# Kernel tuning notes

Hardware: AMD Instinct MI355X
Metric: run time of the kernel (lower is better)

Reference implementation:

```python
import jax, jax.numpy as jnp
import numpy as np
from jax import lax

K = 3
K2 = K * K
EPS = 1e-5


def conv3x3(x, w, b=None):
    # x [B,C,H,W], w [O,C,3,3], padding=1, stride=1
    out = lax.conv_general_dilated(x, w, (1, 1), [(1, 1), (1, 1)],
                                   dimension_numbers=('NCHW', 'OIHW', 'NCHW'))
    if b is not None:
        out = out + b[None, :, None, None]
    return out


def deform_conv(x, w_off, b_off, w_mod, b_mod, w):
    # DCNv2-style deformable conv, k=3, stride=1, pad=1, dilation=1, no bias.
    B, C, H, W = x.shape
    O = w.shape[0]
    off = conv3x3(x, w_off, b_off).reshape(B, K2, 2, H, W)   # (dy,dx) per tap
    mod = 2.0 * jax.nn.sigmoid(conv3x3(x, w_mod, b_mod))      # [B,9,H,W]
    dy, dx = off[:, :, 0], off[:, :, 1]

    ky = (jnp.arange(K) - 1).astype(x.dtype)
    base_y = jnp.repeat(ky, K)   # [9]
    base_x = jnp.tile(ky, K)     # [9]
    ii = jnp.arange(H, dtype=x.dtype)[:, None]
    jj = jnp.arange(W, dtype=x.dtype)[None, :]
    py = ii[None, None] + base_y[None, :, None, None] + dy   # [B,9,H,W]
    px = jj[None, None] + base_x[None, :, None, None] + dx

    def sample(xb, pyb, pxb):
        # xb [C,H,W]; pyb/pxb [9,H,W] -> [C,9,H,W], bilinear w/ zero pad
        y0 = jnp.floor(pyb)
        x0 = jnp.floor(pxb)
        wy = pyb - y0
        wx = pxb - x0
        flat = xb.reshape(C, -1)
        acc = jnp.zeros((C, K2, H, W), xb.dtype)
        for yc, xc, wt in ((y0, x0, (1 - wy) * (1 - wx)),
                           (y0, x0 + 1, (1 - wy) * wx),
                           (y0 + 1, x0, wy * (1 - wx)),
                           (y0 + 1, x0 + 1, wy * wx)):
            yi = yc.astype(jnp.int32)
            xi = xc.astype(jnp.int32)
            valid = (yi >= 0) & (yi < H) & (xi >= 0) & (xi < W)
            idx = (jnp.clip(yi, 0, H - 1) * W + jnp.clip(xi, 0, W - 1)).reshape(-1)
            g = jnp.take(flat, idx, axis=1).reshape(C, K2, H, W)
            acc = acc + g * (wt * valid)[None]
        return acc

    patches = jax.vmap(sample)(x, py, px)          # [B,C,9,H,W]
    patches = patches * mod[:, None]               # modulated
    return jnp.einsum('bckhw,ock->bohw', patches, w.reshape(O, C, K2))


def bn_relu(x):
    # BatchNorm2d(affine=False), train-mode batch stats, biased variance
    mean = jnp.mean(x, axis=(0, 2, 3), keepdims=True)
    var = jnp.mean(jnp.square(x - mean), axis=(0, 2, 3), keepdims=True)
    return jax.nn.relu((x - mean) * lax.rsqrt(var + EPS))


def maxpool2(x):
    return lax.reduce_window(x, -jnp.inf, lax.max, (1, 1, 2, 2), (1, 1, 2, 2), 'VALID')


def setup_inputs() -> dict:
    key = jax.random.key(0)
    ks = jax.random.split(key, 11)
    B, Cin, Cout, H, W = 4, 64, 128, 128, 128
    std1 = 1.0 / np.sqrt(Cin * K2)
    std2 = 1.0 / np.sqrt(Cout * K2)
    return {
        'x': jax.random.normal(ks[0], (B, Cin, H, W), jnp.float32),
        'w_off1': jax.random.normal(ks[1], (2 * K2, Cin, K, K), jnp.float32) * 0.01,
        'b_off1': jax.random.normal(ks[2], (2 * K2,), jnp.float32) * 0.01,
        'w_mod1': jax.random.normal(ks[3], (K2, Cin, K, K), jnp.float32) * 0.01,
        'b_mod1': jnp.zeros((K2,), jnp.float32),
        'w1': jax.random.normal(ks[4], (Cout, Cin, K, K), jnp.float32) * std1,
        'w_off2': jax.random.normal(ks[5], (2 * K2, Cout, K, K), jnp.float32) * 0.01,
        'b_off2': jax.random.normal(ks[6], (2 * K2,), jnp.float32) * 0.01,
        'w_mod2': jax.random.normal(ks[7], (K2, Cout, K, K), jnp.float32) * 0.01,
        'b_mod2': jnp.zeros((K2,), jnp.float32),
        'w2': jax.random.normal(ks[8], (Cout, Cout, K, K), jnp.float32) * std2,
    }


def reference(x, w_off1, b_off1, w_mod1, b_mod1, w1,
              w_off2, b_off2, w_mod2, b_mod2, w2):
    h = bn_relu(deform_conv(x, w_off1, b_off1, w_mod1, b_mod1, w1))
    h = bn_relu(deform_conv(h, w_off2, b_off2, w_mod2, b_mod2, w2))
    return maxpool2(h)
```

## Files before the change

### kernel.cpp

```cpp
#include <hip/hip_runtime.h>
#include <math.h>

#define HH 128
#define WW 128
#define HWSZ 16384

typedef __attribute__((ext_vector_type(8))) _Float16 h8;
typedef __attribute__((ext_vector_type(2))) _Float16 h2;
typedef __attribute__((ext_vector_type(4))) float f32x4;
typedef __attribute__((ext_vector_type(2))) float f32x2;
typedef unsigned short ushort;

__device__ __forceinline__ ushort f2h(float f) {
    _Float16 h = (_Float16)f;
    ushort u;
    __builtin_memcpy(&u, &h, 2);
    return u;
}
__device__ __forceinline__ unsigned f2h2(float lo, float hi) {
    h2 r;
    r.x = (_Float16)lo;
    r.y = (_Float16)hi;
    unsigned u;
    __builtin_memcpy(&u, &r, 4);
    return u;
}
__device__ __forceinline__ f32x2 unpk_h2(unsigned u) {
    h2 h;
    __builtin_memcpy(&h, &u, 4);
    return (f32x2){(float)h.x, (float)h.y};
}

__global__ __launch_bounds__(256) void prep_weights(
    const float* __restrict__ w1, const float* __restrict__ w2,
    const float* __restrict__ w_off1, const float* __restrict__ w_mod1,
    const float* __restrict__ w_off2, const float* __restrict__ w_mod2,
    ushort* __restrict__ Wt1, ushort* __restrict__ Wt2,
    ushort* __restrict__ Wo1, ushort* __restrict__ Wo2) {
    int bid = blockIdx.x, tid = threadIdx.x;
    if (bid < 336) {
        int i = bid * 256 + tid;
        int o = i / 672, kq = i % 672;
        int k = kq / 72, c = kq % 72;
        float v = (k < 9 && c < 64) ? w1[(o * 64 + c) * 9 + k] : 0.f;
        Wt1[i] = f2h(v);
    } else if (bid < 960) {
        int i = (bid - 336) * 256 + tid;
        int o = i / 1248, kq = i % 1248;
        int k = kq / 136, c = kq % 136;
        float v = (k < 9 && c < 128) ? w2[(o * 128 + c) * 9 + k] : 0.f;
        Wt2[i] = f2h(v);
    } else if (bid < 1032) {
        int i = (bid - 960) * 256 + tid;
        int o = i / 576, kap = i % 576;
        int k = kap / 64, c = kap % 64;
        float v = 0.f;
        if (o < 18) v = w_off1[(o * 64 + c) * 9 + k];
        else if (o < 27) v = w_mod1[((o - 18) * 64 + c) * 9 + k];
        Wo1[i] = f2h(v);
    } else {
        int i = (bid - 1032) * 256 + tid;
        int o = i / 1152, kap = i % 1152;
        int k = kap / 128, c = kap % 128;
        float v = 0.f;
        if (o < 18) v = w_off2[(o * 128 + c) * 9 + k];
        else if (o < 27) v = w_mod2[((o - 18) * 128 + c) * 9 + k];
        Wo2[i] = f2h(v);
    }
}

template <int C>
__global__ __launch_bounds__(256) void nhwc_cvt(const float* __restrict__ xin,
                                                unsigned* __restrict__ xout) {
    __shared__ float tile[64][C + 1];
    const int m0 = blockIdx.x * 64;
    const int b = m0 >> 14;
    const int hw0 = m0 & 16383;
    const int t = threadIdx.x;
    const int pr = t & 63, cr = t >> 6;
#pragma unroll
    for (int it = 0; it < C / 4; ++it) {
        int c = it * 4 + cr;
        tile[pr][c] = xin[(((size_t)(b * C + c)) << 14) + hw0 + pr];
    }
    __syncthreads();
    constexpr int CH = C / 2;
#pragma unroll
    for (int it = 0; it < 64 * CH / 256; ++it) {
        int slot = it * 256 + t;
        int p = slot / CH, cc = slot % CH;
        xout[(size_t)(m0 + p) * CH + cc] =
            f2h2(tile[p][2 * cc], tile[p][2 * cc + 1]);
    }
}

__global__ __launch_bounds__(256) void bn_apply_ew(
    const unsigned* __restrict__ xin, const float* __restrict__ praw,
    unsigned* __restrict__ xout) {
    __shared__ float lstats[256];
    if (threadIdx.x < 128) {
        int c = threadIdx.x;
        float s = 0.f, q = 0.f;
#pragma unroll
        for (int r = 0; r < 8; ++r) {
            s += praw[r * 256 + c];
            q += praw[r * 256 + 128 + c];
        }
        float mean = s / 65536.f;
        float var = q / 65536.f - mean * mean;
        lstats[c] = mean;
        lstats[128 + c] = rsqrtf(var + 1e-5f);
    }
    __syncthreads();
    int i = blockIdx.x * 256 + threadIdx.x;
    uint4 v = ((const uint4*)xin)[i];
    int c0 = ((i * 4) & 63) * 2;
    unsigned ov[4];
    unsigned in[4] = {v.x, v.y, v.z, v.w};
#pragma unroll
    for (int d = 0; d < 4; ++d) {
        int c = c0 + 2 * d;
        f32x2 f = unpk_h2(in[d]);
        float a = fmaxf(0.f, (f.x - lstats[c]) * lstats[128 + c]);
        float b2 = fmaxf(0.f, (f.y - lstats[c + 1]) * lstats[128 + c + 1]);
        ov[d] = f2h2(a, b2);
    }
    ((uint4*)xout)[i] = uint4{ov[0], ov[1], ov[2], ov[3]};
}

template <int C>
__global__ __launch_bounds__(256) void offmod_nhwc(
    const ushort* __restrict__ xh, const ushort* __restrict__ wt,
    const float* __restrict__ b_off, const float* __restrict__ b_mod,
    float* __restrict__ dyb, float* __restrict__ dxb, float* __restrict__ mob,
    float* __restrict__ praw) {
    constexpr int K = C * 9;
    if (blockIdx.x < 8) praw[blockIdx.x * 256 + threadIdx.x] = 0.f;
    const int m0 = blockIdx.x * 64;
    const int b = m0 >> 14;
    const int hw0 = m0 & 16383;
    const int h = hw0 >> 7;
    const int w0 = hw0 & 127;
    const int tid = threadIdx.x;
    const int lane = tid & 63, wv = tid >> 6;
    const int n16 = lane & 15, quad = lane >> 4;
    const int p = wv * 16 + n16;
    const int w = w0 + p;

    int tbase[9];
    bool tval[9];
#pragma unroll
    for (int k = 0; k < 9; ++k) {
        int yy = h + k / 3 - 1, xx = w + k % 3 - 1;
        tval[k] = ((unsigned)yy < 128u) && ((unsigned)xx < 128u);
        int cy = min(max(yy, 0), 127), cx = min(max(xx, 0), 127);
        tbase[k] = ((b << 14) + (cy << 7) + cx) * C + quad * 8;
    }

    f32x4 acc[2];
    acc[0] = (f32x4){0.f, 0.f, 0.f, 0.f};
    acc[1] = (f32x4){0.f, 0.f, 0.f, 0.f};

    const ushort* b0p = wt + (size_t)n16 * K + quad * 8;
    const ushort* b1p = wt + (size_t)(16 + n16) * K + quad * 8;

#pragma unroll
    for (int s = 0; s < K / 32; ++s) {
        const int k = (s * 32) / C;
        const int c0 = (s * 32) % C;
        h8 a = {0, 0, 0, 0, 0, 0, 0, 0};
        if (tval[k]) a = *(const h8*)(xh + (size_t)tbase[k] + c0);
        const h8 bv0 = *(const h8*)(b0p + s * 32);
        const h8 bv1 = *(const h8*)(b1p + s * 32);
        acc[0] = __builtin_amdgcn_mfma_f32_16x16x32_f16(a, bv0, acc[0], 0, 0, 0);
        acc[1] = __builtin_amdgcn_mfma_f32_16x16x32_f16(a, bv1, acc[1], 0, 0, 0);
    }

    __shared__ float sm[32 * 65];
#pragma unroll
    for (int nt = 0; nt < 2; ++nt) {
        int n = nt * 16 + n16;
        int pb = wv * 16 + quad * 4;
#pragma unroll
        for (int r = 0; r < 4; ++r) sm[n * 65 + pb + r] = acc[nt][r];
    }
    __syncthreads();
    {
        int n = tid >> 3, i8 = tid & 7;
        if (n < 27) {
            const float* sp = sm + n * 65 + i8 * 8;
            int px = hw0 + i8 * 8;
            if (n < 18) {
                int k = n >> 1;
                float bias = b_off[n];
                float* dst =
                    ((n & 1) ? dxb : dyb) + (((size_t)(b * 9 + k)) << 14) + px;
#pragma unroll
                for (int j = 0; j < 8; j += 4) {
                    float4 v = make_float4(sp[j] + bias, sp[j + 1] + bias,
                                           sp[j + 2] + bias, sp[j + 3] + bias);
                    *(float4*)(dst + j) = v;
                }
            } else {
                float bias = b_mod[n - 18];
                float* dst = mob + (((size_t)(b * 9 + (n - 18))) << 14) + px;
#pragma unroll
                for (int j = 0; j < 8; j += 4) {
                    float4 v;
                    v.x = 2.f / (1.f + expf(-(sp[j] + bias)));
                    v.y = 2.f / (1.f + expf(-(sp[j + 1] + bias)));
                    v.z = 2.f / (1.f + expf(-(sp[j + 2] + bias)));
                    v.w = 2.f / (1.f + expf(-(sp[j + 3] + bias)));
                    *(float4*)(dst + j) = v;
                }
            }
        }
    }
}

template <int C>
__global__ __launch_bounds__(256) void deform_mfma3(
    const ushort* __restrict__ xh, const float* __restrict__ dyb,
    const float* __restrict__ dxb, const float* __restrict__ mob,
    const ushort* __restrict__ wt, unsigned* __restrict__ xout,
    float* __restrict__ praw) {
    constexpr int PIX = 32;
    constexpr int AST = C + 8;
    constexpr int CPW = C + 8;
    constexpr int KP = ((9 * CPW + 31) / 32) * 32;
    constexpr int NCC = C / 8;
    constexpr int NIT = PIX * NCC / 256;
    constexpr int ABUF = PIX * AST;

    __shared__ __align__(16) char smem_raw[2 * ABUF * 2 + PIX * 9 * 32];
    ushort* abuf0 = (ushort*)smem_raw;
    ushort* abuf1 = abuf0 + ABUF;
    int* tb = (int*)(abuf0 + 2 * ABUF);
    float* tw = (float*)(tb + PIX * 9 * 4);

    const int m0 = blockIdx.x * PIX;
    const int b = m0 >> 14;
    const int hw0 = m0 & 16383;
    const int h = hw0 >> 7, w0 = hw0 & 127;
    const int tid = threadIdx.x;

    for (int r = tid; r < PIX * 9; r += 256) {
        int p = r & (PIX - 1), k = r / PIX;
        int oi = ((b * 9 + k) << 14) + hw0 + p;
        float py = (float)(h + k / 3 - 1) + dyb[oi];
        float px = (float)(w0 + p + k % 3 - 1) + dxb[oi];
        float mv = mob[oi];
        float y0f = floorf(py), x0f = floorf(px);
        float wy = py - y0f, wx = px - x0f;
        int y0 = (int)y0f, x0 = (int)x0f;
        int y1 = y0 + 1, x1 = x0 + 1;
        float f00 = (1.f - wy) * (1.f - wx) *
                    (((unsigned)y0 < 128u && (unsigned)x0 < 128u) ? mv : 0.f);
        float f01 = (1.f - wy) * wx *
                    (((unsigned)y0 < 128u && (unsigned)x1 < 128u) ? mv : 0.f);
        float f10 = wy * (1.f - wx) *
                    (((unsigned)y1 < 128u && (unsigned)x0 < 128u) ? mv : 0.f);
        float f11 = wy * wx *
                    (((unsigned)y1 < 128u && (unsigned)x1 < 128u) ? mv : 0.f);
        int cy0 = min(max(y0, 0), 127), cy1 = min(max(y1, 0), 127);
        int cx0 = min(max(x0, 0), 127), cx1 = min(max(x1, 0), 127);
        int bpx = b << 14;
        int s = (p * 9 + k) * 4;
        tb[s + 0] = (bpx + (cy0 << 7) + cx0) * C;
        tb[s + 1] = (bpx + (cy0 << 7) + cx1) * C;
        tb[s + 2] = (bpx + (cy1 << 7) + cx0) * C;
        tb[s + 3] = (bpx + (cy1 << 7) + cx1) * C;
        tw[s + 0] = f00;
        tw[s + 1] = f01;
        tw[s + 2] = f10;
        tw[s + 3] = f11;
    }
    __syncthreads();

    auto issue_loads = [&](int kc, uint4 (&q)[2][4], float4 (&fw)[2]) {
#pragma unroll
        for (int it = 0; it < NIT; ++it) {
            int e = it * 256 + tid;
            int p = e / NCC, cc = e % NCC;
            int s = (p * 9 + kc) * 4;
            int4 bi = *(const int4*)&tb[s];
            fw[it] = *(const float4*)&tw[s];
            q[it][0] = *(const uint4*)(xh + (size_t)bi.x + cc * 8);
            q[it][1] = *(const uint4*)(xh + (size_t)bi.y + cc * 8);
            q[it][2] = *(const uint4*)(xh + (size_t)bi.z + cc * 8);
            q[it][3] = *(const uint4*)(xh + (size_t)bi.w + cc * 8);
        }
    };
    auto interp_write = [&](ushort* dst, uint4 (&q)[2][4], float4 (&fw)[2]) {
#pragma unroll
        for (int it = 0; it < NIT; ++it) {
            int e = it * 256 + tid;
            int p = e / NCC, cc = e % NCC;
            _Float16 w0h = (_Float16)fw[it].x, w1h = (_Float16)fw[it].y;
            _Float16 w2h = (_Float16)fw[it].z, w3h = (_Float16)fw[it].w;
            h8 F0 = {w0h, w0h, w0h, w0h, w0h, w0h, w0h, w0h};
            h8 F1 = {w1h, w1h, w1h, w1h, w1h, w1h, w1h, w1h};
            h8 F2 = {w2h, w2h, w2h, w2h, w2h, w2h, w2h, w2h};
            h8 F3 = {w3h, w3h, w3h, w3h, w3h, w3h, w3h, w3h};
            h8 a0, a1, a2, a3;
            __builtin_memcpy(&a0, &q[it][0], 16);
            __builtin_memcpy(&a1, &q[it][1], 16);
            __builtin_memcpy(&a2, &q[it][2], 16);
            __builtin_memcpy(&a3, &q[it][3], 16);
            h8 v = a0 * F0 + a1 * F1 + a2 * F2 + a3 * F3;
            uint4 ov;
            __builtin_memcpy(&ov, &v, 16);
            *(uint4*)&dst[p * AST + cc * 8] = ov;
        }
    };

    {
        uint4 q[2][4];
        float4 fw[2];
        issue_loads(0, q, fw);
        interp_write(abuf0, q, fw);
    }
    __syncthreads();

    const int lane = tid & 63, wv = tid >> 6;
    const int n16 = lane & 15, quad = lane >> 4;

    f32x4 acc[2][2];
#pragma unroll
    for (int mt = 0; mt < 2; ++mt)
#pragma unroll
        for (int nt = 0; nt < 2; ++nt) acc[mt][nt] = (f32x4){0.f, 0.f, 0.f, 0.f};

    const ushort* bbase[2];
#pragma unroll
    for (int nt = 0; nt < 2; ++nt)
        bbase[nt] = wt + (size_t)(wv * 32 + nt * 16 + n16) * KP + quad * 8;

#pragma unroll 1
    for (int kc = 0; kc < 9; ++kc) {
        uint4 q[2][4];
        float4 fw[2];
        if (kc < 8) issue_loads(kc + 1, q, fw);

        const ushort* ab = (kc & 1) ? abuf1 : abuf0;
#pragma unroll
        for (int s = 0; s < C / 32; ++s) {
            h8 av[2], bv[2];
#pragma unroll
            for (int mt = 0; mt < 2; ++mt)
                av[mt] = *(const h8*)(ab + (mt * 16 + n16) * AST + s * 32 +
                                      quad * 8);
#pragma unroll
            for (int nt = 0; nt < 2; ++nt)
                bv[nt] = *(const h8*)(bbase[nt] + kc * CPW + s * 32);
#pragma unroll
            for (int mt = 0; mt < 2; ++mt)
#pragma unroll
                for (int nt = 0; nt < 2; ++nt)
                    acc[mt][nt] = __builtin_amdgcn_mfma_f32_16x16x32_f16(
                        av[mt], bv[nt], acc[mt][nt], 0, 0, 0);
        }
        if (kc < 8)
            interp_write((kc & 1) ? abuf0 : abuf1, q, fw);
        __syncthreads();
    }

    float* sm = (float*)smem_raw;
    constexpr int SROW = PIX + 1;
#pragma unroll
    for (int mt = 0; mt < 2; ++mt)
#pragma unroll
        for (int nt = 0; nt < 2; ++nt) {
            int o = wv * 32 + nt * 16 + n16;
            int mb = mt * 16 + quad * 4;
#pragma unroll
            for (int r = 0; r < 4; ++r) sm[o * SROW + mb + r] = acc[mt][nt][r];
        }
    __syncthreads();
    {
        int o = tid >> 1, half = tid & 1;
        const float* sp = sm + o * SROW + half * 16;
        float s = 0.f, qq = 0.f;
#pragma unroll
        for (int i = 0; i < 16; i += 4) {
            float4 v = make_float4(sp[i], sp[i + 1], sp[i + 2], sp[i + 3]);
            s += v.x + v.y + v.z + v.w;
            qq += v.x * v.x + v.y * v.y + v.z * v.z + v.w * v.w;
        }
        s += __shfl_down(s, 1, 64);
        qq += __shfl_down(qq, 1, 64);
        if (half == 0) {
            float* pr = praw + (blockIdx.x & 7) * 256;
            atomicAdd(&pr[o], s);
            atomicAdd(&pr[128 + o], qq);
        }
    }
    {
        int p = tid >> 3, cc8 = tid & 7;
        unsigned ov[8];
#pragma unroll
        for (int j = 0; j < 8; ++j) {
            int c = cc8 * 16 + 2 * j;
            ov[j] = f2h2(sm[c * SROW + p], sm[(c + 1) * SROW + p]);
        }
        uint4* dst = (uint4*)(xout + ((size_t)(m0 + p)) * 64 + cc8 * 8);
        dst[0] = uint4{ov[0], ov[1], ov[2], ov[3]};
        dst[1] = uint4{ov[4], ov[5], ov[6], ov[7]};
    }
}

template <int C>
__global__ __launch_bounds__(256) void deform_mfma3p(
    const ushort* __restrict__ xh, const float* __restrict__ dyb,
    const float* __restrict__ dxb, const float* __restrict__ mob,
    const ushort* __restrict__ wt, float* __restrict__ pout,
    float* __restrict__ praw) {
    constexpr int PIX = 32;
    constexpr int AST = C + 8;
    constexpr int CPW = C + 8;
    constexpr int KP = ((9 * CPW + 31) / 32) * 32;
    constexpr int NCC = C / 8;
    constexpr int NIT = PIX * NCC / 256;
    constexpr int ABUF = PIX * AST;

    __shared__ __align__(16) char smem_raw[2 * ABUF * 2 + PIX * 9 * 32];
    ushort* abuf0 = (ushort*)smem_raw;
    ushort* abuf1 = abuf0 + ABUF;
    int* tb = (int*)(abuf0 + 2 * ABUF);
    float* tw = (float*)(tb + PIX * 9 * 4);

    const int bid = blockIdx.x;
    const int b = bid >> 9;
    const int rp = (bid >> 3) & 63;
    const int g = bid & 7;
    const int tid = threadIdx.x;

    for (int r = tid; r < PIX * 9; r += 256) {
        int p = r & (PIX - 1), k = r / PIX;
        int row = 2 * rp + (p >> 4), col = g * 16 + (p & 15);
        int oi = ((b * 9 + k) << 14) + (row << 7) + col;
        float py = (float)(row + k / 3 - 1) + dyb[oi];
        float px = (float)(col + k % 3 - 1) + dxb[oi];
        float mv = mob[oi];
        float y0f = floorf(py), x0f = floorf(px);
        float wy = py - y0f, wx = px - x0f;
        int y0 = (int)y0f, x0 = (int)x0f;
        int y1 = y0 + 1, x1 = x0 + 1;
        float f00 = (1.f - wy) * (1.f - wx) *
                    (((unsigned)y0 < 128u && (unsigned)x0 < 128u) ? mv : 0.f);
        float f01 = (1.f - wy) * wx *
                    (((unsigned)y0 < 128u && (unsigned)x1 < 128u) ? mv : 0.f);
        float f10 = wy * (1.f - wx) *
                    (((unsigned)y1 < 128u && (unsigned)x0 < 128u) ? mv : 0.f);
        float f11 = wy * wx *
                    (((unsigned)y1 < 128u && (unsigned)x1 < 128u) ? mv : 0.f);
        int cy0 = min(max(y0, 0), 127), cy1 = min(max(y1, 0), 127);
        int cx0 = min(max(x0, 0), 127), cx1 = min(max(x1, 0), 127);
        int bpx = b << 14;
        int s = (p * 9 + k) * 4;
        tb[s + 0] = (bpx + (cy0 << 7) + cx0) * C;
        tb[s + 1] = (bpx + (cy0 << 7) + cx1) * C;
        tb[s + 2] = (bpx + (cy1 << 7) + cx0) * C;
        tb[s + 3] = (bpx + (cy1 << 7) + cx1) * C;
        tw[s + 0] = f00;
        tw[s + 1] = f01;
        tw[s + 2] = f10;
        tw[s + 3] = f11;
    }
    __syncthreads();

    auto issue_loads = [&](int kc, uint4 (&q)[2][4], float4 (&fw)[2]) {
#pragma unroll
        for (int it = 0; it < NIT; ++it) {
            int e = it * 256 + tid;
            int p = e / NCC, cc = e % NCC;
            int s = (p * 9 + kc) * 4;
            int4 bi = *(const int4*)&tb[s];
            fw[it] = *(const float4*)&tw[s];
            q[it][0] = *(const uint4*)(xh + (size_t)bi.x + cc * 8);
            q[it][1] = *(const uint4*)(xh + (size_t)bi.y + cc * 8);
            q[it][2] = *(const uint4*)(xh + (size_t)bi.z + cc * 8);
            q[it][3] = *(const uint4*)(xh + (size_t)bi.w + cc * 8);
        }
    };
    auto interp_write = [&](ushort* dst, uint4 (&q)[2][4], float4 (&fw)[2]) {
#pragma unroll
        for (int it = 0; it < NIT; ++it) {
            int e = it * 256 + tid;
            int p = e / NCC, cc = e % NCC;
            _Float16 w0h = (_Float16)fw[it].x, w1h = (_Float16)fw[it].y;
            _Float16 w2h = (_Float16)fw[it].z, w3h = (_Float16)fw[it].w;
            h8 F0 = {w0h, w0h, w0h, w0h, w0h, w0h, w0h, w0h};
            h8 F1 = {w1h, w1h, w1h, w1h, w1h, w1h, w1h, w1h};
            h8 F2 = {w2h, w2h, w2h, w2h, w2h, w2h, w2h, w2h};
            h8 F3 = {w3h, w3h, w3h, w3h, w3h, w3h, w3h, w3h};
            h8 a0, a1, a2, a3;
            __builtin_memcpy(&a0, &q[it][0], 16);
            __builtin_memcpy(&a1, &q[it][1], 16);
            __builtin_memcpy(&a2, &q[it][2], 16);
            __builtin_memcpy(&a3, &q[it][3], 16);
            h8 v = a0 * F0 + a1 * F1 + a2 * F2 + a3 * F3;
            uint4 ov;
            __builtin_memcpy(&ov, &v, 16);
            *(uint4*)&dst[p * AST + cc * 8] = ov;
        }
    };

    {
        uint4 q[2][4];
        float4 fw[2];
        issue_loads(0, q, fw);
        interp_write(abuf0, q, fw);
    }
    __syncthreads();

    const int lane = tid & 63, wv = tid >> 6;
    const int n16 = lane & 15, quad = lane >> 4;

    f32x4 acc[2][2];
#pragma unroll
    for (int mt = 0; mt < 2; ++mt)
#pragma unroll
        for (int nt = 0; nt < 2; ++nt) acc[mt][nt] = (f32x4){0.f, 0.f, 0.f, 0.f};

    const ushort* bbase[2];
#pragma unroll
    for (int nt = 0; nt < 2; ++nt)
        bbase[nt] = wt + (size_t)(wv * 32 + nt * 16 + n16) * KP + quad * 8;

#pragma unroll 1
    for (int kc = 0; kc < 9; ++kc) {
        uint4 q[2][4];
        float4 fw[2];
        if (kc < 8) issue_loads(kc + 1, q, fw);

        const ushort* ab = (kc & 1) ? abuf1 : abuf0;
#pragma unroll
        for (int s = 0; s < C / 32; ++s) {
            h8 av[2], bv[2];
#pragma unroll
            for (int mt = 0; mt < 2; ++mt)
                av[mt] = *(const h8*)(ab + (mt * 16 + n16) * AST + s * 32 +
                                      quad * 8);
#pragma unroll
            for (int nt = 0; nt < 2; ++nt)
                bv[nt] = *(const h8*)(bbase[nt] + kc * CPW + s * 32);
#pragma unroll
            for (int mt = 0; mt < 2; ++mt)
#pragma unroll
                for (int nt = 0; nt < 2; ++nt)
                    acc[mt][nt] = __builtin_amdgcn_mfma_f32_16x16x32_f16(
                        av[mt], bv[nt], acc[mt][nt], 0, 0, 0);
        }
        if (kc < 8)
            interp_write((kc & 1) ? abuf0 : abuf1, q, fw);
        __syncthreads();
    }

    float* sm = (float*)smem_raw;
    constexpr int SROW = PIX + 1;
#pragma unroll
    for (int mt = 0; mt < 2; ++mt)
#pragma unroll
        for (int nt = 0; nt < 2; ++nt) {
            int o = wv * 32 + nt * 16 + n16;
            int mb = mt * 16 + quad * 4;
#pragma unroll
            for (int r = 0; r < 4; ++r) sm[o * SROW + mb + r] = acc[mt][nt][r];
        }
    __syncthreads();
    {
        int o = tid >> 1, half = tid & 1;
        const float* so = sm + o * SROW;
        const float* sp = so + half * 16;
        float s = 0.f, qq = 0.f;
#pragma unroll
        for (int i = 0; i < 16; i += 4) {
            float4 v = make_float4(sp[i], sp[i + 1], sp[i + 2], sp[i + 3]);
            s += v.x + v.y + v.z + v.w;
            qq += v.x * v.x + v.y * v.y + v.z * v.z + v.w * v.w;
        }
        s += __shfl_down(s, 1, 64);
        qq += __shfl_down(qq, 1, 64);
        if (half == 0) {
            float* pr = praw + (blockIdx.x & 7) * 256;
            atomicAdd(&pr[o], s);
            atomicAdd(&pr[128 + o], qq);
        }
        float4 pv;
#pragma unroll
        for (int i = 0; i < 4; ++i) {
            int pc = half * 4 + i;
            float m0v = fmaxf(so[2 * pc], so[2 * pc + 1]);
            float m1v = fmaxf(so[16 + 2 * pc], so[16 + 2 * pc + 1]);
            ((float*)&pv)[i] = fmaxf(m0v, m1v);
        }
        *(float4*)(pout + (((size_t)(b * 128 + o)) << 12) + rp * 64 + g * 8 +
                   half * 4) = pv;
    }
}

__global__ __launch_bounds__(256) void pool_norm(const float* __restrict__ pout,
                                                 const float* __restrict__ praw,
                                                 float* __restrict__ out) {
    __shared__ float lstats[256];
    if (threadIdx.x < 128) {
        int c = threadIdx.x;
        float s = 0.f, q = 0.f;
#pragma unroll
        for (int r = 0; r < 8; ++r) {
            s += praw[r * 256 + c];
            q += praw[r * 256 + 128 + c];
        }
        float mean = s / 65536.f;
        float var = q / 65536.f - mean * mean;
        lstats[c] = mean;
        lstats[128 + c] = rsqrtf(var + 1e-5f);
    }
    __syncthreads();
    int i = blockIdx.x * 256 + threadIdx.x;
    int c = (i >> 10) & 127;
    float mean = lstats[c], rstd = lstats[128 + c];
    float4 v = ((const float4*)pout)[i];
    v.x = fmaxf(0.f, (v.x - mean) * rstd);
    v.y = fmaxf(0.f, (v.y - mean) * rstd);
    v.z = fmaxf(0.f, (v.z - mean) * rstd);
    v.w = fmaxf(0.f, (v.w - mean) * rstd);
    ((float4*)out)[i] = v;
}

extern "C" void kernel_launch(void* const* d_in, const int* in_sizes, int n_in,
                              void* d_out, int out_size, void* d_ws,
                              size_t ws_size, hipStream_t stream) {
    (void)in_sizes;
    (void)n_in;
    (void)out_size;
    (void)ws_size;
    const float* x = (const float*)d_in[0];
    const float* w_off1 = (const float*)d_in[1];
    const float* b_off1 = (const float*)d_in[2];
    const float* w_mod1 = (const float*)d_in[3];
    const float* b_mod1 = (const float*)d_in[4];
    const float* w1 = (const float*)d_in[5];
    const float* w_off2 = (const float*)d_in[6];
    const float* b_off2 = (const float*)d_in[7];
    const float* w_mod2 = (const float*)d_in[8];
    const float* b_mod2 = (const float*)d_in[9];
    const float* w2 = (const float*)d_in[10];
    float* out = (float*)d_out;
    float* ws = (float*)d_ws;

    ushort* Wt1 = (ushort*)ws;
    ushort* Wt2 = (ushort*)(ws + 43008);
    ushort* Wo1 = (ushort*)(ws + 43008 + 79872);
    ushort* Wo2 = (ushort*)(ws + 43008 + 79872 + 16384);
    float* dyb = ws + 172032;
    float* dxb = dyb + 589824;
    float* mob = dxb + 589824;
    float* hbuf = mob + 589824;
    float* xhf = hbuf + 8388608;
    float* h1hf = xhf + 2097152;
    float* praw = h1hf + 4194304;
    ushort* xh = (ushort*)xhf;
    ushort* h1h = (ushort*)h1hf;

    prep_weights<<<1176, 256, 0, stream>>>(w1, w2, w_off1, w_mod1, w_off2,
                                           w_mod2, Wt1, Wt2, Wo1, Wo2);

    nhwc_cvt<64><<<1024, 256, 0, stream>>>(x, (unsigned*)xh);
    offmod_nhwc<64><<<1024, 256, 0, stream>>>(xh, Wo1, b_off1, b_mod1, dyb, dxb,
                                              mob, praw);
    deform_mfma3<64><<<2048, 256, 0, stream>>>(xh, dyb, dxb, mob, Wt1,
                                               (unsigned*)hbuf, praw);
    bn_apply_ew<<<4096, 256, 0, stream>>>((const unsigned*)hbuf, praw,
                                          (unsigned*)h1h);

    offmod_nhwc<128><<<1024, 256, 0, stream>>>(h1h, Wo2, b_off2, b_mod2, dyb,
                                               dxb, mob, praw);
    deform_mfma3p<128><<<2048, 256, 0, stream>>>(h1h, dyb, dxb, mob, Wt2, hbuf,
                                                 praw);
    pool_norm<<<2048, 256, 0, stream>>>(hbuf, praw, out);
}
```

Measured before the change: 276.7 us.

## Double pixel tile per block, compress gather tables, swizzle LDS, split pipeline

Both deformable-conv MFMA kernels now process 64 pixels per block instead of 32, so each wave issues 4x2 MFMA tiles and reuses each weight fragment across twice as many rows. The launch grid halves to match. The per-tap gather table shrinks to one packed base offset with neighbour flags plus fp16-packed bilinear weights. LDS padding is replaced by an XOR swizzle. The gather/interpolate stage is split into two halves interleaved with the MFMA halves to overlap global loads with compute. This costs more registers and LDS per block, under a launch bound of 4 blocks per CU, and the weights now lose precision earlier by being stored as fp16.

```diff
diff --git a/kernel.cpp b/kernel.cpp
--- a/kernel.cpp
+++ b/kernel.cpp
@@ -219,33 +219,41 @@
 }
 
 template <int C>
-__global__ __launch_bounds__(256) void deform_mfma3(
+__global__ __launch_bounds__(256, 4) void deform_mfma3(
     const ushort* __restrict__ xh, const float* __restrict__ dyb,
     const float* __restrict__ dxb, const float* __restrict__ mob,
     const ushort* __restrict__ wt, unsigned* __restrict__ xout,
     float* __restrict__ praw) {
-    constexpr int PIX = 32;
-    constexpr int AST = C + 8;
+    constexpr int PIX = 64;
+    constexpr int NCH = C / 8;
+    constexpr int NCC = C / 8;
+    constexpr int NIT = PIX * NCC / 256;
+    constexpr int HNIT = NIT / 2;
+    constexpr int SH = (C / 32) / 2 > 0 ? (C / 32) / 2 : 1;
     constexpr int CPW = C + 8;
     constexpr int KP = ((9 * CPW + 31) / 32) * 32;
-    constexpr int NCC = C / 8;
-    constexpr int NIT = PIX * NCC / 256;
-    constexpr int ABUF = PIX * AST;
-
-    __shared__ __align__(16) char smem_raw[2 * ABUF * 2 + PIX * 9 * 32];
+    constexpr int ABUF = PIX * C;
+    constexpr int LOOPB = 2 * ABUF * 2 + PIX * 9 * 4 + PIX * 9 * 8;
+    constexpr int EPIB = 128 * (PIX + 1) * 4;
+    constexpr int SMEMB = LOOPB > EPIB ? LOOPB : EPIB;
+
+    __shared__ __align__(16) char smem_raw[SMEMB];
     ushort* abuf0 = (ushort*)smem_raw;
     ushort* abuf1 = abuf0 + ABUF;
-    int* tb = (int*)(abuf0 + 2 * ABUF);
-    float* tw = (float*)(tb + PIX * 9 * 4);
+    int* tbl = (int*)(abuf0 + 2 * ABUF);
+    unsigned* twl = (unsigned*)(smem_raw + 2 * ABUF * 2 + PIX * 9 * 4);
 
     const int m0 = blockIdx.x * PIX;
     const int b = m0 >> 14;
     const int hw0 = m0 & 16383;
     const int h = hw0 >> 7, w0 = hw0 & 127;
     const int tid = threadIdx.x;
+    const int lane = tid & 63, wv = tid >> 6;
+    const int n16 = lane & 15, quad = lane >> 4;
+    const int xr = n16 & (NCH - 1);
 
     for (int r = tid; r < PIX * 9; r += 256) {
-        int p = r & (PIX - 1), k = r / PIX;
+        int p = r & (PIX - 1), k = r >> 6;
         int oi = ((b * 9 + k) << 14) + hw0 + p;
         float py = (float)(h + k / 3 - 1) + dyb[oi];
         float px = (float)(w0 + p + k % 3 - 1) + dxb[oi];
@@ -264,70 +272,63 @@
                     (((unsigned)y1 < 128u && (unsigned)x1 < 128u) ? mv : 0.f);
         int cy0 = min(max(y0, 0), 127), cy1 = min(max(y1, 0), 127);
         int cx0 = min(max(x0, 0), 127), cx1 = min(max(x1, 0), 127);
-        int bpx = b << 14;
-        int s = (p * 9 + k) * 4;
-        tb[s + 0] = (bpx + (cy0 << 7) + cx0) * C;
-        tb[s + 1] = (bpx + (cy0 << 7) + cx1) * C;
-        tb[s + 2] = (bpx + (cy1 << 7) + cx0) * C;
-        tb[s + 3] = (bpx + (cy1 << 7) + cx1) * C;
-        tw[s + 0] = f00;
-        tw[s + 1] = f01;
-        tw[s + 2] = f10;
-        tw[s + 3] = f11;
-    }
-    __syncthreads();
-
-    auto issue_loads = [&](int kc, uint4 (&q)[2][4], float4 (&fw)[2]) {
-#pragma unroll
-        for (int it = 0; it < NIT; ++it) {
-            int e = it * 256 + tid;
+        int base00 = (((b << 14) + (cy0 << 7) + cx0)) * C;
+        int flags = ((cy1 != cy0) ? 2 : 0) | ((cx1 != cx0) ? 1 : 0);
+        int s = p * 9 + k;
+        tbl[s] = base00 | flags;
+        twl[2 * s] = f2h2(f00, f01);
+        twl[2 * s + 1] = f2h2(f10, f11);
+    }
+    __syncthreads();
+
+    auto issue_loads = [&](int kc, int it0, uint4 (&q)[HNIT][4],
+                           uint2 (&fw)[HNIT]) {
+#pragma unroll
+        for (int j = 0; j < HNIT; ++j) {
+            int e = (it0 + j) * 256 + tid;
             int p = e / NCC, cc = e % NCC;
-            int s = (p * 9 + kc) * 4;
-            int4 bi = *(const int4*)&tb[s];
-            fw[it] = *(const float4*)&tw[s];
-            q[it][0] = *(const uint4*)(xh + (size_t)bi.x + cc * 8);
-            q[it][1] = *(const uint4*)(xh + (size_t)bi.y + cc * 8);
-            q[it][2] = *(const uint4*)(xh + (size_t)bi.z + cc * 8);
-            q[it][3] = *(const uint4*)(xh + (size_t)bi.w + cc * 8);
+            int s = p * 9 + kc;
+            int ent = tbl[s];
+            fw[j] = *(const uint2*)&twl[2 * s];
+            int base = ent & ~3;
+            int dxo = (ent & 1) ? C : 0;
+            int dyo = (ent & 2) ? (C << 7) : 0;
+            const ushort* pp = xh + (size_t)base + cc * 8;
+            q[j][0] = *(const uint4*)(pp);
+            q[j][1] = *(const uint4*)(pp + dxo);
+            q[j][2] = *(const uint4*)(pp + dyo);
+            q[j][3] = *(const uint4*)(pp + dyo + dxo);
         }
     };
-    auto interp_write = [&](ushort* dst, uint4 (&q)[2][4], float4 (&fw)[2]) {
-#pragma unroll
-        for (int it = 0; it < NIT; ++it) {
-            int e = it * 256 + tid;
+    auto interp_write = [&](ushort* dst, int it0, uint4 (&q)[HNIT][4],
+                            uint2 (&fw)[HNIT]) {
+#pragma unroll
+        for (int j = 0; j < HNIT; ++j) {
+            int e = (it0 + j) * 256 + tid;
             int p = e / NCC, cc = e % NCC;
-            _Float16 w0h = (_Float16)fw[it].x, w1h = (_Float16)fw[it].y;
-            _Float16 w2h = (_Float16)fw[it].z, w3h = (_Float16)fw[it].w;
-            h8 F0 = {w0h, w0h, w0h, w0h, w0h, w0h, w0h, w0h};
-            h8 F1 = {w1h, w1h, w1h, w1h, w1h, w1h, w1h, w1h};
-            h8 F2 = {w2h, w2h, w2h, w2h, w2h, w2h, w2h, w2h};
-            h8 F3 = {w3h, w3h, w3h, w3h, w3h, w3h, w3h, w3h};
+            h2 w01, w23;
+            __builtin_memcpy(&w01, &fw[j].x, 4);
+            __builtin_memcpy(&w23, &fw[j].y, 4);
+            h8 F0 = {w01.x, w01.x, w01.x, w01.x, w01.x, w01.x, w01.x, w01.x};
+            h8 F1 = {w01.y, w01.y, w01.y, w01.y, w01.y, w01.y, w01.y, w01.y};
+            h8 F2 = {w23.x, w23.x, w23.x, w23.x, w23.x, w23.x, w23.x, w23.x};
+            h8 F3 = {w23.y, w23.y, w23.y, w23.y, w23.y, w23.y, w23.y, w23.y};
             h8 a0, a1, a2, a3;
-            __builtin_memcpy(&a0, &q[it][0], 16);
-            __builtin_memcpy(&a1, &q[it][1], 16);
-            __builtin_memcpy(&a2, &q[it][2], 16);
-            __builtin_memcpy(&a3, &q[it][3], 16);
+            __builtin_memcpy(&a0, &q[j][0], 16);
+            __builtin_memcpy(&a1, &q[j][1], 16);
+            __builtin_memcpy(&a2, &q[j][2], 16);
+            __builtin_memcpy(&a3, &q[j][3], 16);
             h8 v = a0 * F0 + a1 * F1 + a2 * F2 + a3 * F3;
             uint4 ov;
             __builtin_memcpy(&ov, &v, 16);
-            *(uint4*)&dst[p * AST + cc * 8] = ov;
+            int ccs = cc ^ (p & (NCH - 1));
+            *(uint4*)&dst[p * C + ccs * 8] = ov;
         }
     };
 
-    {
-        uint4 q[2][4];
-        float4 fw[2];
-        issue_loads(0, q, fw);
-        interp_write(abuf0, q, fw);
-    }
-    __syncthreads();
-
-    const int lane = tid & 63, wv = tid >> 6;
-    const int n16 = lane & 15, quad = lane >> 4;
-
-    f32x4 acc[2][2];
-#pragma unroll
-    for (int mt = 0; mt < 2; ++mt)
+    f32x4 acc[4][2];
+#pragma unroll
+    for (int mt = 0; mt < 4; ++mt)
 #pragma unroll
         for (int nt = 0; nt < 2; ++nt) acc[mt][nt] = (f32x4){0.f, 0.f, 0.f, 0.f};
 
@@ -336,39 +337,57 @@
     for (int nt = 0; nt < 2; ++nt)
         bbase[nt] = wt + (size_t)(wv * 32 + nt * 16 + n16) * KP + quad * 8;
 
-#pragma unroll 1
-    for (int kc = 0; kc < 9; ++kc) {
-        uint4 q[2][4];
-        float4 fw[2];
-        if (kc < 8) issue_loads(kc + 1, q, fw);
-
-        const ushort* ab = (kc & 1) ? abuf1 : abuf0;
-#pragma unroll
-        for (int s = 0; s < C / 32; ++s) {
-            h8 av[2], bv[2];
-#pragma unroll
-            for (int mt = 0; mt < 2; ++mt)
-                av[mt] = *(const h8*)(ab + (mt * 16 + n16) * AST + s * 32 +
-                                      quad * 8);
+    auto mfma_run = [&](const ushort* ab, int kc, int s0, int s1) {
+#pragma unroll
+        for (int s = s0; s < s1; ++s) {
+            h8 av[4], bv[2];
+            int ch = (s * 4 + quad) ^ xr;
+#pragma unroll
+            for (int mt = 0; mt < 4; ++mt)
+                av[mt] = *(const h8*)(ab + (mt * 16 + n16) * C + ch * 8);
 #pragma unroll
             for (int nt = 0; nt < 2; ++nt)
                 bv[nt] = *(const h8*)(bbase[nt] + kc * CPW + s * 32);
 #pragma unroll
-            for (int mt = 0; mt < 2; ++mt)
+            for (int mt = 0; mt < 4; ++mt)
 #pragma unroll
                 for (int nt = 0; nt < 2; ++nt)
                     acc[mt][nt] = __builtin_amdgcn_mfma_f32_16x16x32_f16(
                         av[mt], bv[nt], acc[mt][nt], 0, 0, 0);
         }
-        if (kc < 8)
-            interp_write((kc & 1) ? abuf0 : abuf1, q, fw);
+    };
+
+    {
+        uint4 q[HNIT][4];
+        uint2 fw[HNIT];
+        issue_loads(0, 0, q, fw);
+        interp_write(abuf0, 0, q, fw);
+        issue_loads(0, HNIT, q, fw);
+        interp_write(abuf0, HNIT, q, fw);
+    }
+    __syncthreads();
+
+#pragma unroll 1
+    for (int kc = 0; kc < 9; ++kc) {
+        const ushort* ab = (kc & 1) ? abuf1 : abuf0;
+        ushort* dst = (kc & 1) ? abuf0 : abuf1;
+        uint4 q[HNIT][4];
+        uint2 fw[HNIT];
+        if (kc < 8) issue_loads(kc + 1, 0, q, fw);
+        mfma_run(ab, kc, 0, SH);
+        if (kc < 8) {
+            interp_write(dst, 0, q, fw);
+            issue_loads(kc + 1, HNIT, q, fw);
+        }
+        mfma_run(ab, kc, SH, C / 32);
+        if (kc < 8) interp_write(dst, HNIT, q, fw);
         __syncthreads();
     }
 
     float* sm = (float*)smem_raw;
     constexpr int SROW = PIX + 1;
 #pragma unroll
-    for (int mt = 0; mt < 2; ++mt)
+    for (int mt = 0; mt < 4; ++mt)
 #pragma unroll
         for (int nt = 0; nt < 2; ++nt) {
             int o = wv * 32 + nt * 16 + n16;
@@ -379,10 +398,10 @@
     __syncthreads();
     {
         int o = tid >> 1, half = tid & 1;
-        const float* sp = sm + o * SROW + half * 16;
+        const float* sp = sm + o * SROW + half * 32;
         float s = 0.f, qq = 0.f;
 #pragma unroll
-        for (int i = 0; i < 16; i += 4) {
+        for (int i = 0; i < 32; i += 4) {
             float4 v = make_float4(sp[i], sp[i + 1], sp[i + 2], sp[i + 3]);
             s += v.x + v.y + v.z + v.w;
             qq += v.x * v.x + v.y * v.y + v.z * v.z + v.w * v.w;
@@ -396,48 +415,58 @@
         }
     }
     {
-        int p = tid >> 3, cc8 = tid & 7;
-        unsigned ov[8];
-#pragma unroll
-        for (int j = 0; j < 8; ++j) {
-            int c = cc8 * 16 + 2 * j;
+        int p = tid >> 2, cc4 = tid & 3;
+        unsigned ov[16];
+#pragma unroll
+        for (int j = 0; j < 16; ++j) {
+            int c = cc4 * 32 + 2 * j;
             ov[j] = f2h2(sm[c * SROW + p], sm[(c + 1) * SROW + p]);
         }
-        uint4* dst = (uint4*)(xout + ((size_t)(m0 + p)) * 64 + cc8 * 8);
+        uint4* dst = (uint4*)(xout + ((size_t)(m0 + p)) * 64 + cc4 * 16);
         dst[0] = uint4{ov[0], ov[1], ov[2], ov[3]};
         dst[1] = uint4{ov[4], ov[5], ov[6], ov[7]};
+        dst[2] = uint4{ov[8], ov[9], ov[10], ov[11]};
+        dst[3] = uint4{ov[12], ov[13], ov[14], ov[15]};
     }
 }
 
 template <int C>
-__global__ __launch_bounds__(256) void deform_mfma3p(
+__global__ __launch_bounds__(256, 4) void deform_mfma3p(
     const ushort* __restrict__ xh, const float* __restrict__ dyb,
     const float* __restrict__ dxb, const float* __restrict__ mob,
     const ushort* __restrict__ wt, float* __restrict__ pout,
     float* __restrict__ praw) {
-    constexpr int PIX = 32;
-    constexpr int AST = C + 8;
+    constexpr int PIX = 64;
+    constexpr int NCH = C / 8;
+    constexpr int NCC = C / 8;
+    constexpr int NIT = PIX * NCC / 256;
+    constexpr int HNIT = NIT / 2;
+    constexpr int SH = (C / 32) / 2 > 0 ? (C / 32) / 2 : 1;
     constexpr int CPW = C + 8;
     constexpr int KP = ((9 * CPW + 31) / 32) * 32;
-    constexpr int NCC = C / 8;
-    constexpr int NIT = PIX * NCC / 256;
-    constexpr int ABUF = PIX * AST;
-
-    __shared__ __align__(16) char smem_raw[2 * ABUF * 2 + PIX * 9 * 32];
+    constexpr int ABUF = PIX * C;
+    constexpr int LOOPB = 2 * ABUF * 2 + PIX * 9 * 4 + PIX * 9 * 8;
+    constexpr int EPIB = 128 * (PIX + 1) * 4;
+    constexpr int SMEMB = LOOPB > EPIB ? LOOPB : EPIB;
+
+    __shared__ __align__(16) char smem_raw[SMEMB];
     ushort* abuf0 = (ushort*)smem_raw;
     ushort* abuf1 = abuf0 + ABUF;
-    int* tb = (int*)(abuf0 + 2 * ABUF);
-    float* tw = (float*)(tb + PIX * 9 * 4);
+    int* tbl = (int*)(abuf0 + 2 * ABUF);
+    unsigned* twl = (unsigned*)(smem_raw + 2 * ABUF * 2 + PIX * 9 * 4);
 
     const int bid = blockIdx.x;
-    const int b = bid >> 9;
-    const int rp = (bid >> 3) & 63;
-    const int g = bid & 7;
+    const int b = bid >> 8;
+    const int rp = (bid >> 2) & 63;
+    const int g = bid & 3;
     const int tid = threadIdx.x;
+    const int lane = tid & 63, wv = tid >> 6;
+    const int n16 = lane & 15, quad = lane >> 4;
+    const int xr = n16 & (NCH - 1);
 
     for (int r = tid; r < PIX * 9; r += 256) {
-        int p = r & (PIX - 1), k = r / PIX;
-        int row = 2 * rp + (p >> 4), col = g * 16 + (p & 15);
+        int p = r & (PIX - 1), k = r >> 6;
+        int row = 2 * rp + (p >> 5), col = g * 32 + (p & 31);
         int oi = ((b * 9 + k) << 14) + (row << 7) + col;
         float py = (float)(row + k / 3 - 1) + dyb[oi];
         float px = (float)(col + k % 3 - 1) + dxb[oi];
@@ -456,70 +485,63 @@
                     (((unsigned)y1 < 128u && (unsigned)x1 < 128u) ? mv : 0.f);
         int cy0 = min(max(y0, 0), 127), cy1 = min(max(y1, 0), 127);
         int cx0 = min(max(x0, 0), 127), cx1 = min(max(x1, 0), 127);
-        int bpx = b << 14;
-        int s = (p * 9 + k) * 4;
-        tb[s + 0] = (bpx + (cy0 << 7) + cx0) * C;
-        tb[s + 1] = (bpx + (cy0 << 7) + cx1) * C;
-        tb[s + 2] = (bpx + (cy1 << 7) + cx0) * C;
-        tb[s + 3] = (bpx + (cy1 << 7) + cx1) * C;
-        tw[s + 0] = f00;
-        tw[s + 1] = f01;
-        tw[s + 2] = f10;
-        tw[s + 3] = f11;
-    }
-    __syncthreads();
-
-    auto issue_loads = [&](int kc, uint4 (&q)[2][4], float4 (&fw)[2]) {
-#pragma unroll
-        for (int it = 0; it < NIT; ++it) {
-            int e = it * 256 + tid;
+        int base00 = (((b << 14) + (cy0 << 7) + cx0)) * C;
+        int flags = ((cy1 != cy0) ? 2 : 0) | ((cx1 != cx0) ? 1 : 0);
+        int s = p * 9 + k;
+        tbl[s] = base00 | flags;
+        twl[2 * s] = f2h2(f00, f01);
+        twl[2 * s + 1] = f2h2(f10, f11);
+    }
+    __syncthreads();
+
+    auto issue_loads = [&](int kc, int it0, uint4 (&q)[HNIT][4],
+                           uint2 (&fw)[HNIT]) {
+#pragma unroll
+        for (int j = 0; j < HNIT; ++j) {
+            int e = (it0 + j) * 256 + tid;
             int p = e / NCC, cc = e % NCC;
-            int s = (p * 9 + kc) * 4;
-            int4 bi = *(const int4*)&tb[s];
-            fw[it] = *(const float4*)&tw[s];
-            q[it][0] = *(const uint4*)(xh + (size_t)bi.x + cc * 8);
-            q[it][1] = *(const uint4*)(xh + (size_t)bi.y + cc * 8);
-            q[it][2] = *(const uint4*)(xh + (size_t)bi.z + cc * 8);
-            q[it][3] = *(const uint4*)(xh + (size_t)bi.w + cc * 8);
+            int s = p * 9 + kc;
+            int ent = tbl[s];
+            fw[j] = *(const uint2*)&twl[2 * s];
+            int base = ent & ~3;
+            int dxo = (ent & 1) ? C : 0;
+            int dyo = (ent & 2) ? (C << 7) : 0;
+            const ushort* pp = xh + (size_t)base + cc * 8;
+            q[j][0] = *(const uint4*)(pp);
+            q[j][1] = *(const uint4*)(pp + dxo);
+            q[j][2] = *(const uint4*)(pp + dyo);
+            q[j][3] = *(const uint4*)(pp + dyo + dxo);
         }
     };
-    auto interp_write = [&](ushort* dst, uint4 (&q)[2][4], float4 (&fw)[2]) {
-#pragma unroll
-        for (int it = 0; it < NIT; ++it) {
-            int e = it * 256 + tid;
+    auto interp_write = [&](ushort* dst, int it0, uint4 (&q)[HNIT][4],
+                            uint2 (&fw)[HNIT]) {
+#pragma unroll
+        for (int j = 0; j < HNIT; ++j) {
+            int e = (it0 + j) * 256 + tid;
             int p = e / NCC, cc = e % NCC;
-            _Float16 w0h = (_Float16)fw[it].x, w1h = (_Float16)fw[it].y;
-            _Float16 w2h = (_Float16)fw[it].z, w3h = (_Float16)fw[it].w;
-            h8 F0 = {w0h, w0h, w0h, w0h, w0h, w0h, w0h, w0h};
-            h8 F1 = {w1h, w1h, w1h, w1h, w1h, w1h, w1h, w1h};
-            h8 F2 = {w2h, w2h, w2h, w2h, w2h, w2h, w2h, w2h};
-            h8 F3 = {w3h, w3h, w3h, w3h, w3h, w3h, w3h, w3h};
+            h2 w01, w23;
+            __builtin_memcpy(&w01, &fw[j].x, 4);
+            __builtin_memcpy(&w23, &fw[j].y, 4);
+            h8 F0 = {w01.x, w01.x, w01.x, w01.x, w01.x, w01.x, w01.x, w01.x};
+            h8 F1 = {w01.y, w01.y, w01.y, w01.y, w01.y, w01.y, w01.y, w01.y};
+            h8 F2 = {w23.x, w23.x, w23.x, w23.x, w23.x, w23.x, w23.x, w23.x};
+            h8 F3 = {w23.y, w23.y, w23.y, w23.y, w23.y, w23.y, w23.y, w23.y};
             h8 a0, a1, a2, a3;
-            __builtin_memcpy(&a0, &q[it][0], 16);
-            __builtin_memcpy(&a1, &q[it][1], 16);
-            __builtin_memcpy(&a2, &q[it][2], 16);
-            __builtin_memcpy(&a3, &q[it][3], 16);
+            __builtin_memcpy(&a0, &q[j][0], 16);
+            __builtin_memcpy(&a1, &q[j][1], 16);
+            __builtin_memcpy(&a2, &q[j][2], 16);
+            __builtin_memcpy(&a3, &q[j][3], 16);
             h8 v = a0 * F0 + a1 * F1 + a2 * F2 + a3 * F3;
             uint4 ov;
             __builtin_memcpy(&ov, &v, 16);
-            *(uint4*)&dst[p * AST + cc * 8] = ov;
+            int ccs = cc ^ (p & (NCH - 1));
+            *(uint4*)&dst[p * C + ccs * 8] = ov;
         }
     };
 
-    {
-        uint4 q[2][4];
-        float4 fw[2];
-        issue_loads(0, q, fw);
-        interp_write(abuf0, q, fw);
-    }
-    __syncthreads();
-
-    const int lane = tid & 63, wv = tid >> 6;
-    const int n16 = lane & 15, quad = lane >> 4;
-
-    f32x4 acc[2][2];
-#pragma unroll
-    for (int mt = 0; mt < 2; ++mt)
+    f32x4 acc[4][2];
+#pragma unroll
+    for (int mt = 0; mt < 4; ++mt)
 #pragma unroll
         for (int nt = 0; nt < 2; ++nt) acc[mt][nt] = (f32x4){0.f, 0.f, 0.f, 0.f};
 
@@ -528,39 +550,57 @@
     for (int nt = 0; nt < 2; ++nt)
         bbase[nt] = wt + (size_t)(wv * 32 + nt * 16 + n16) * KP + quad * 8;
 
-#pragma unroll 1
-    for (int kc = 0; kc < 9; ++kc) {
-        uint4 q[2][4];
-        float4 fw[2];
-        if (kc < 8) issue_loads(kc + 1, q, fw);
-
-        const ushort* ab = (kc & 1) ? abuf1 : abuf0;
-#pragma unroll
-        for (int s = 0; s < C / 32; ++s) {
-            h8 av[2], bv[2];
-#pragma unroll
-            for (int mt = 0; mt < 2; ++mt)
-                av[mt] = *(const h8*)(ab + (mt * 16 + n16) * AST + s * 32 +
-                                      quad * 8);
+    auto mfma_run = [&](const ushort* ab, int kc, int s0, int s1) {
+#pragma unroll
+        for (int s = s0; s < s1; ++s) {
+            h8 av[4], bv[2];
+            int ch = (s * 4 + quad) ^ xr;
+#pragma unroll
+            for (int mt = 0; mt < 4; ++mt)
+                av[mt] = *(const h8*)(ab + (mt * 16 + n16) * C + ch * 8);
 #pragma unroll
             for (int nt = 0; nt < 2; ++nt)
                 bv[nt] = *(const h8*)(bbase[nt] + kc * CPW + s * 32);
 #pragma unroll
-            for (int mt = 0; mt < 2; ++mt)
+            for (int mt = 0; mt < 4; ++mt)
 #pragma unroll
                 for (int nt = 0; nt < 2; ++nt)
                     acc[mt][nt] = __builtin_amdgcn_mfma_f32_16x16x32_f16(
                         av[mt], bv[nt], acc[mt][nt], 0, 0, 0);
         }
-        if (kc < 8)
-            interp_write((kc & 1) ? abuf0 : abuf1, q, fw);
+    };
+
+    {
+        uint4 q[HNIT][4];
+        uint2 fw[HNIT];
+        issue_loads(0, 0, q, fw);
+        interp_write(abuf0, 0, q, fw);
+        issue_loads(0, HNIT, q, fw);
+        interp_write(abuf0, HNIT, q, fw);
+    }
+    __syncthreads();
+
+#pragma unroll 1
+    for (int kc = 0; kc < 9; ++kc) {
+        const ushort* ab = (kc & 1) ? abuf1 : abuf0;
+        ushort* dst = (kc & 1) ? abuf0 : abuf1;
+        uint4 q[HNIT][4];
+        uint2 fw[HNIT];
+        if (kc < 8) issue_loads(kc + 1, 0, q, fw);
+        mfma_run(ab, kc, 0, SH);
+        if (kc < 8) {
+            interp_write(dst, 0, q, fw);
+            issue_loads(kc + 1, HNIT, q, fw);
+        }
+        mfma_run(ab, kc, SH, C / 32);
+        if (kc < 8) interp_write(dst, HNIT, q, fw);
         __syncthreads();
     }
 
     float* sm = (float*)smem_raw;
     constexpr int SROW = PIX + 1;
 #pragma unroll
-    for (int mt = 0; mt < 2; ++mt)
+    for (int mt = 0; mt < 4; ++mt)
 #pragma unroll
         for (int nt = 0; nt < 2; ++nt) {
             int o = wv * 32 + nt * 16 + n16;
@@ -572,10 +612,10 @@
     {
         int o = tid >> 1, half = tid & 1;
         const float* so = sm + o * SROW;
-        const float* sp = so + half * 16;
+        const float* sp = so + half * 32;
         float s = 0.f, qq = 0.f;
 #pragma unroll
-        for (int i = 0; i < 16; i += 4) {
+        for (int i = 0; i < 32; i += 4) {
             float4 v = make_float4(sp[i], sp[i + 1], sp[i + 2], sp[i + 3]);
             s += v.x + v.y + v.z + v.w;
             qq += v.x * v.x + v.y * v.y + v.z * v.z + v.w * v.w;
@@ -587,16 +627,20 @@
             atomicAdd(&pr[o], s);
             atomicAdd(&pr[128 + o], qq);
         }
-        float4 pv;
-#pragma unroll
-        for (int i = 0; i < 4; ++i) {
-            int pc = half * 4 + i;
+        float4 pv0, pv1;
+#pragma unroll
+        for (int i = 0; i < 8; ++i) {
+            int pc = half * 8 + i;
             float m0v = fmaxf(so[2 * pc], so[2 * pc + 1]);
-            float m1v = fmaxf(so[16 + 2 * pc], so[16 + 2 * pc + 1]);
-            ((float*)&pv)[i] = fmaxf(m0v, m1v);
-        }
-        *(float4*)(pout + (((size_t)(b * 128 + o)) << 12) + rp * 64 + g * 8 +
-                   half * 4) = pv;
+            float m1v = fmaxf(so[32 + 2 * pc], so[32 + 2 * pc + 1]);
+            float m = fmaxf(m0v, m1v);
+            if (i < 4) ((float*)&pv0)[i] = m;
+            else ((float*)&pv1)[i - 4] = m;
+        }
+        float* dp = pout + (((size_t)(b * 128 + o)) << 12) + rp * 64 + g * 16 +
+                    half * 8;
+        *(float4*)(dp) = pv0;
+        *(float4*)(dp + 4) = pv1;
     }
 }
 
@@ -670,14 +714,14 @@
     nhwc_cvt<64><<<1024, 256, 0, stream>>>(x, (unsigned*)xh);
     offmod_nhwc<64><<<1024, 256, 0, stream>>>(xh, Wo1, b_off1, b_mod1, dyb, dxb,
                                               mob, praw);
-    deform_mfma3<64><<<2048, 256, 0, stream>>>(xh, dyb, dxb, mob, Wt1,
+    deform_mfma3<64><<<1024, 256, 0, stream>>>(xh, dyb, dxb, mob, Wt1,
                                                (unsigned*)hbuf, praw);
     bn_apply_ew<<<4096, 256, 0, stream>>>((const unsigned*)hbuf, praw,
                                           (unsigned*)h1h);
 
     offmod_nhwc<128><<<1024, 256, 0, stream>>>(h1h, Wo2, b_off2, b_mod2, dyb,
                                                dxb, mob, praw);
-    deform_mfma3p<128><<<2048, 256, 0, stream>>>(h1h, dyb, dxb, mob, Wt2, hbuf,
+    deform_mfma3p<128><<<1024, 256, 0, stream>>>(h1h, dyb, dxb, mob, Wt2, hbuf,
                                                  praw);
     pool_norm<<<2048, 256, 0, stream>>>(hbuf, praw, out);
 }
```

After: 255.2 us. 7.8% less time.
